# Performance work log

Hardware: AMD Instinct MI355X
Metric: run time of the kernel (lower is better)

Reference implementation:

```python
import jax, jax.numpy as jnp
import numpy as np

H = 32          # num_attention_heads
HD = 128        # head_dim
HID = H * HD    # hidden_size = 4096
KB_LEN = 1024   # number of KB entries
TOPK = 128      # top_k_kb (dynamic_sparsify=True)
ROPE_THETA = 10000.0
PAD = -1000000000.0  # PADDING_VALUE


def rope_cos_sin(position_ids, head_dim, theta):
    inv_freq = 1.0 / (theta ** (jnp.arange(0, head_dim, 2, dtype=jnp.float32) / head_dim))
    freqs = position_ids.astype(jnp.float32)[..., None] * inv_freq  # [B,q,hd/2]
    emb = jnp.concatenate([freqs, freqs], axis=-1)                  # [B,q,hd]
    return jnp.cos(emb), jnp.sin(emb)


def rotate_half(x):
    half = x.shape[-1] // 2
    return jnp.concatenate([-x[..., half:], x[..., :half]], axis=-1)


def apply_rope(q, k, cos, sin):
    cos = cos[:, None]  # [B,1,q,hd]
    sin = sin[:, None]
    return q * cos + rotate_half(q) * sin, k * cos + rotate_half(k) * sin


def setup_inputs() -> dict:
    key = jax.random.key(0)
    ks = jax.random.split(key, 9)
    B, Q = 1, 2048
    w_scale = 0.02  # keep activations numerically sane
    hidden_states = jax.random.normal(ks[0], (B, Q, HID), jnp.float32)
    causal = jnp.where(jnp.tril(jnp.ones((Q, Q), bool)), 0.0, PAD).astype(jnp.float32)
    attention_mask = jnp.broadcast_to(causal[None, None], (B, 1, Q, Q))
    position_ids = jnp.broadcast_to(jnp.arange(Q)[None], (B, Q))
    kb_keys = jax.random.normal(ks[1], (KB_LEN, HID), jnp.float32)
    kb_values = jax.random.normal(ks[2], (KB_LEN, HID), jnp.float32)
    Wq = jax.random.normal(ks[3], (HID, HID), jnp.float32) * w_scale
    Wq2 = jax.random.normal(ks[4], (HID, HID), jnp.float32) * w_scale
    Wk = jax.random.normal(ks[5], (HID, HID), jnp.float32) * w_scale
    Wv = jax.random.normal(ks[6], (HID, HID), jnp.float32) * w_scale
    Wo = jax.random.normal(ks[7], (HID, HID), jnp.float32) * w_scale
    score_shift = jnp.zeros((H, 1), jnp.float32) - 3.0
    return {"hidden_states": hidden_states, "attention_mask": attention_mask,
            "position_ids": position_ids, "kb_keys": kb_keys, "kb_values": kb_values,
            "Wq": Wq, "Wq2": Wq2, "Wk": Wk, "Wv": Wv, "Wo": Wo,
            "score_shift": score_shift}


def kblam_attention(hidden_states, attention_mask, position_ids, kb_keys, kb_values,
                    Wq, Wq2, Wk, Wv, Wo, score_shift):
    B, Q, _ = hidden_states.shape
    scale = 1.0 / np.sqrt(HD)

    def heads(x):  # [B,Q,HID] -> [B,H,Q,HD]
        return x.reshape(B, Q, H, HD).transpose(0, 2, 1, 3)

    q = heads(hidden_states @ Wq.T)
    q2 = heads(hidden_states @ Wq2.T)   # second query head (used for KB top-k pruning)
    k = heads(hidden_states @ Wk.T)
    v = heads(hidden_states @ Wv.T)

    cos, sin = rope_cos_sin(position_ids, HD, ROPE_THETA)
    q, k = apply_rope(q, k, cos, sin)   # num_kv_groups == 1, repeat_kv is identity

    # --- KB path: [kb_len, H*HD] -> [B,H,kb_len,HD] ---
    kbk = jnp.broadcast_to(kb_keys.reshape(KB_LEN, H, HD).transpose(1, 0, 2)[None], (B, H, KB_LEN, HD))
    kbv = jnp.broadcast_to(kb_values.reshape(KB_LEN, H, HD).transpose(1, 0, 2)[None], (B, H, KB_LEN, HD))

    # prune_key_value (dynamic_sparsify): top-k KB rows by summed q2-scores
    aw2 = jnp.einsum('bhqd,bhkd->bhqk', q2, kbk) * scale          # [B,H,Q,KB_LEN]
    idx = jax.lax.stop_gradient(jax.lax.top_k(aw2.sum((1, 2)), TOPK)[1])  # [B,TOPK]
    gidx = jnp.broadcast_to(idx[:, None, :, None], (B, H, TOPK, HD))
    kbk = jnp.take_along_axis(kbk, gidx, axis=2)                  # [B,H,TOPK,HD]
    kbv = jnp.take_along_axis(kbv, gidx, axis=2)
    kb_len = TOPK

    k_all = jnp.concatenate([kbk, k], axis=2)                     # [B,H,kb_len+Q,HD]
    v_all = jnp.concatenate([kbv, v], axis=2)

    # kb attention mask: zeros, except fully-padded query rows get PADDING_VALUE
    padding_mask = jnp.all(attention_mask < 0, axis=-1, keepdims=True)  # [B,1,Q,1]
    kb_mask = jnp.where(padding_mask, PAD, 0.0).astype(attention_mask.dtype)
    mask = jnp.concatenate([jnp.broadcast_to(kb_mask, (B, 1, Q, kb_len)), attention_mask], axis=-1)

    attn = jnp.einsum('bhqd,bhkd->bhqk', q, k_all) * scale
    # learned per-head shift on KB scores (score_shift: [H,1], init -3)
    attn = attn.at[..., :kb_len].add(score_shift.reshape(1, H, 1, 1))
    attn = attn + mask
    attn = jax.nn.softmax(attn.astype(jnp.float32), axis=-1).astype(q.dtype)

    out = jnp.einsum('bhqk,bhkd->bhqd', attn, v_all)              # [B,H,Q,HD]
    out = out.transpose(0, 2, 1, 3).reshape(B, Q, HID)
    return out @ Wo.T


def reference(hidden_states, attention_mask, position_ids, kb_keys, kb_values,
              Wq, Wq2, Wk, Wv, Wo, score_shift):
    return kblam_attention(hidden_states, attention_mask, position_ids, kb_keys, kb_values,
                           Wq, Wq2, Wk, Wv, Wo, score_shift)
```

## Files before the change

### kernel.cpp

```cpp
#include <hip/hip_runtime.h>
#include <stdint.h>
#include <stddef.h>

#define NH 32
#define HD 128
#define HID 4096
#define QLEN 2048
#define KBLEN 1024
#define NTOPK 128
#define KVLEN 2176
#define PADV -1e9f
#define SCALE 0.08838834764831845f
#define LOG2E 1.4426950408889634f
#define SC2 (SCALE * LOG2E)
#define DEFER_THR 8.0f

typedef __attribute__((ext_vector_type(4))) float f32x4;
typedef __attribute__((ext_vector_type(4))) unsigned short u16x4;
typedef __attribute__((ext_vector_type(8))) short s16x8;

typedef const __attribute__((address_space(1))) void* gas1_t;
typedef __attribute__((address_space(3))) void* las3_t;

__device__ __forceinline__ void gload_lds16(const void* g, void* l) {
  __builtin_amdgcn_global_load_lds((gas1_t)g, (las3_t)l, 16, 0, 0);
}

__device__ __forceinline__ unsigned short f2bf(float x) {
  union { float f; unsigned u; } z; z.f = x;
  unsigned r = z.u + 0x7fffu + ((z.u >> 16) & 1u);
  return (unsigned short)(r >> 16);
}


__global__ void k_cast(const float* __restrict__ src, unsigned short* __restrict__ dst, int n4) {
  int i = blockIdx.x * 256 + threadIdx.x;
  if (i >= n4) return;
  f32x4 v = ((const f32x4*)src)[i];
  u16x4 o;
  o[0] = f2bf(v[0]); o[1] = f2bf(v[1]); o[2] = f2bf(v[2]); o[3] = f2bf(v[3]);
  ((u16x4*)dst)[i] = o;
}

__global__ void k_rowsum_p(const float* __restrict__ x, float* __restrict__ part) {
  int d = blockIdx.x * 256 + threadIdx.x;
  int q0 = blockIdx.y * 128;
  float acc = 0.f;
  for (int q = q0; q < q0 + 128; ++q) acc += x[(size_t)q * HID + d];
  part[(size_t)blockIdx.y * HID + d] = acc;
}
__global__ void k_rowsum_r(const float* __restrict__ part, float* __restrict__ out) {
  int d = blockIdx.x * 256 + threadIdx.x;
  float acc = 0.f;
#pragma unroll
  for (int i = 0; i < 16; ++i) acc += part[(size_t)i * HID + d];
  out[d] = acc;
}

__global__ void k_dotrows(const float* __restrict__ vec, const float* __restrict__ mat,
                          float* __restrict__ out, int K, float s) {
  int n = blockIdx.x * 4 + (threadIdx.x >> 6);
  int lane = threadIdx.x & 63;
  const float* row = mat + (size_t)n * K;
  float acc = 0.f;
  for (int j = lane; j < K; j += 64) acc += vec[j] * row[j];
#pragma unroll
  for (int off = 32; off > 0; off >>= 1) acc += __shfl_down(acc, off, 64);
  if (lane == 0) out[n] = acc * s;
}

__global__ void k_topk(const float* __restrict__ scores, int* __restrict__ idx) {
  __shared__ float s[KBLEN];
  int t = threadIdx.x;
  s[t] = scores[t];
  __syncthreads();
  float mine = s[t];
  int rank = 0;
  for (int j = 0; j < KBLEN; ++j) {
    float v = s[j];
    rank += (v > mine) || (v == mine && j < t);
  }
  if (rank < NTOPK) idx[rank] = t;
}

__global__ void k_cs(const int* __restrict__ pos_ids, float2* __restrict__ cs) {
  int t = blockIdx.x * 256 + threadIdx.x;
  int p = t >> 6, i = t & 63;
  float pos = (float)pos_ids[p];
  float invf = powf(10000.0f, -(float)i / 64.0f);
  float a = pos * invf;
  cs[p * 64 + i] = make_float2(cosf(a), sinf(a));
}

__global__ void k_gather(const float* __restrict__ kbk, const float* __restrict__ kbv,
                         const int* __restrict__ idx,
                         unsigned short* __restrict__ kall, unsigned short* __restrict__ vallT) {
  int t = blockIdx.x * 256 + threadIdx.x;
  int d = t & 127;
  int i = (t >> 7) & 127;
  int hh = t >> 14;
  int kr = idx[i];
  size_t src = (size_t)kr * HID + hh * HD + d;
  kall[((size_t)hh * KVLEN + i) * HD + d] = f2bf(kbk[src]);
  vallT[((size_t)hh * HD + d) * KVLEN + i] = f2bf(kbv[src]);
}

#define GBK 64
#define ABUF 8192
#define BBUF 16384
#define BUFE (ABUF + BBUF)

template<int MODE>
__global__ __launch_bounds__(512)
void gemm_bt(const unsigned short* __restrict__ A, const unsigned short* __restrict__ B,
             float* __restrict__ Cf, unsigned short* __restrict__ Cb,
             int M, int N, int K, int RH, int RO, const float2* __restrict__ cs2) {
  __shared__ unsigned short lds[3 * BUFE];
  const int tid = threadIdx.x;
  const int lane = tid & 63;
  const int wave = tid >> 6;
  const int lo = lane & 15, hi = lane >> 4;
  const int wm = wave >> 2, wn = wave & 3;

  const int nwg = gridDim.x * gridDim.y;
  const int orig = blockIdx.y * gridDim.x + blockIdx.x;
  const int wg = (orig & 7) * (nwg >> 3) + (orig >> 3);
  const int bx = wg % gridDim.x, by = wg / gridDim.x;
  const int m0 = by * 128, n0 = bx * 256;

  auto stageA = [&](int kt, int bufe, int g) {
    int j0 = g * 512 + wave * 64;
    int j = j0 + lane;
    int row = j >> 3, cb = j & 7;
    gload_lds16(A + (size_t)(m0 + row) * K + kt * GBK + ((cb ^ (row & 7)) << 3),
                (void*)(lds + bufe + j0 * 8));
  };
  auto stageB = [&](int kt, int bufe, int g) {
    int j0 = g * 512 + wave * 64;
    int j = j0 + lane;
    int row = j >> 3, cb = j & 7;
    gload_lds16(B + (size_t)(n0 + row) * K + kt * GBK + ((cb ^ (row & 7)) << 3),
                (void*)(lds + bufe + ABUF + j0 * 8));
  };

  f32x4 acc[4][4] = {};

  stageA(0, 0, 0); stageA(0, 0, 1);
  stageB(0, 0, 0); stageB(0, 0, 1); stageB(0, 0, 2); stageB(0, 0, 3);
  stageA(1, BUFE, 0); stageA(1, BUFE, 1);
  stageB(1, BUFE, 0); stageB(1, BUFE, 1); stageB(1, BUFE, 2); stageB(1, BUFE, 3);

  const int NT = K / GBK;
  const int sa = (lo & 7) << 3;
  const int bbase = (wn >> 1) * 128 + (wn & 1) * 32;
  int bi = 0;

  for (int kt = 0; kt < NT; ++kt) {
    if (kt < NT - 1) { asm volatile("s_waitcnt vmcnt(6)" ::: "memory"); }
    else             { asm volatile("s_waitcnt vmcnt(0)" ::: "memory"); }
    __builtin_amdgcn_sched_barrier(0);
    __builtin_amdgcn_s_barrier();
    __builtin_amdgcn_sched_barrier(0);

    const int bufe = bi * BUFE;
    const int nbufe = ((bi + 2 >= 3) ? bi - 1 : bi + 2) * BUFE;
    const bool pre = (kt + 2 < NT);
    const unsigned short* Ab = lds + bufe;
    const unsigned short* Bb = lds + bufe + ABUF;
    const int arow = wm * 64 + lo;
    const int brow = bbase + lo;

    s16x8 af[4], b01[2], b23[2];
    const int c0 = (hi * 8) ^ sa;
    const int c1 = (32 + hi * 8) ^ sa;

#pragma unroll
    for (int i = 0; i < 4; ++i) af[i] = *(const s16x8*)(Ab + (arow + i * 16) * 64 + c0);
    b01[0] = *(const s16x8*)(Bb + (brow +  0) * 64 + c0);
    b01[1] = *(const s16x8*)(Bb + (brow + 16) * 64 + c0);
    if (pre) { stageA(kt + 2, nbufe, 0); stageA(kt + 2, nbufe, 1); }
    asm volatile("s_waitcnt lgkmcnt(0)" ::: "memory");
    __builtin_amdgcn_sched_barrier(0);
    __builtin_amdgcn_s_setprio(1);
#pragma unroll
    for (int i = 0; i < 4; ++i) {
      acc[i][0] = __builtin_amdgcn_mfma_f32_16x16x32_bf16(af[i], b01[0], acc[i][0], 0, 0, 0);
      acc[i][1] = __builtin_amdgcn_mfma_f32_16x16x32_bf16(af[i], b01[1], acc[i][1], 0, 0, 0);
    }
    __builtin_amdgcn_s_setprio(0);

    b23[0] = *(const s16x8*)(Bb + (brow + 64) * 64 + c0);
    b23[1] = *(const s16x8*)(Bb + (brow + 80) * 64 + c0);
    if (pre) { stageB(kt + 2, nbufe, 0); stageB(kt + 2, nbufe, 1); }
    asm volatile("s_waitcnt lgkmcnt(0)" ::: "memory");
    __builtin_amdgcn_sched_barrier(0);
    __builtin_amdgcn_s_setprio(1);
#pragma unroll
    for (int i = 0; i < 4; ++i) {
      acc[i][2] = __builtin_amdgcn_mfma_f32_16x16x32_bf16(af[i], b23[0], acc[i][2], 0, 0, 0);
      acc[i][3] = __builtin_amdgcn_mfma_f32_16x16x32_bf16(af[i], b23[1], acc[i][3], 0, 0, 0);
    }
    __builtin_amdgcn_s_setprio(0);

#pragma unroll
    for (int i = 0; i < 4; ++i) af[i] = *(const s16x8*)(Ab + (arow + i * 16) * 64 + c1);
    b01[0] = *(const s16x8*)(Bb + (brow +  0) * 64 + c1);
    b01[1] = *(const s16x8*)(Bb + (brow + 16) * 64 + c1);
    if (pre) { stageB(kt + 2, nbufe, 2); stageB(kt + 2, nbufe, 3); }
    asm volatile("s_waitcnt lgkmcnt(0)" ::: "memory");
    __builtin_amdgcn_sched_barrier(0);
    __builtin_amdgcn_s_setprio(1);
#pragma unroll
    for (int i = 0; i < 4; ++i) {
      acc[i][0] = __builtin_amdgcn_mfma_f32_16x16x32_bf16(af[i], b01[0], acc[i][0], 0, 0, 0);
      acc[i][1] = __builtin_amdgcn_mfma_f32_16x16x32_bf16(af[i], b01[1], acc[i][1], 0, 0, 0);
    }
    __builtin_amdgcn_s_setprio(0);

    b23[0] = *(const s16x8*)(Bb + (brow + 64) * 64 + c1);
    b23[1] = *(const s16x8*)(Bb + (brow + 80) * 64 + c1);
    asm volatile("s_waitcnt lgkmcnt(0)" ::: "memory");
    __builtin_amdgcn_sched_barrier(0);
    __builtin_amdgcn_s_setprio(1);
#pragma unroll
    for (int i = 0; i < 4; ++i) {
      acc[i][2] = __builtin_amdgcn_mfma_f32_16x16x32_bf16(af[i], b23[0], acc[i][2], 0, 0, 0);
      acc[i][3] = __builtin_amdgcn_mfma_f32_16x16x32_bf16(af[i], b23[1], acc[i][3], 0, 0, 0);
    }
    __builtin_amdgcn_s_setprio(0);

    bi = (bi + 1 == 3) ? 0 : bi + 1;
  }

  if (MODE == 2) {
#pragma unroll
    for (int i = 0; i < 4; ++i) {
#pragma unroll
      for (int j = 0; j < 2; ++j) {
#pragma unroll
        for (int r = 0; r < 4; ++r) {
          int row = m0 + wm * 64 + i * 16 + hi * 4 + r;
          int col = n0 + bbase + j * 16 + lo;
          int hh = col >> 7, d = col & 127;
          float2 cp = cs2[row * 64 + d];
          float x1 = acc[i][j][r], x2 = acc[i][j + 2][r];
          size_t base = ((size_t)hh * RH + RO + row) * HD;
          Cb[base + d]      = f2bf(x1 * cp.x - x2 * cp.y);
          Cb[base + d + 64] = f2bf(x2 * cp.x + x1 * cp.y);
        }
      }
    }
  } else if (MODE == 3) {
#pragma unroll
    for (int i = 0; i < 4; ++i) {
#pragma unroll
      for (int j = 0; j < 4; ++j) {
        int rowb = m0 + wm * 64 + i * 16 + hi * 4;
        int col = n0 + bbase + (j >> 1) * 64 + (j & 1) * 16 + lo;
        int hh = col >> 7, d = col & 127;
        u16x4 o4;
#pragma unroll
        for (int r = 0; r < 4; ++r) o4[r] = f2bf(acc[i][j][r]);
        *(u16x4*)(Cb + ((size_t)hh * HD + d) * RH + RO + rowb) = o4;
      }
    }
  } else {
#pragma unroll
    for (int i = 0; i < 4; ++i) {
#pragma unroll
      for (int j = 0; j < 4; ++j) {
#pragma unroll
        for (int r = 0; r < 4; ++r) {
          int row = m0 + wm * 64 + i * 16 + hi * 4 + r;
          int col = n0 + bbase + (j >> 1) * 64 + (j & 1) * 16 + lo;
          float v = acc[i][j][r];
          if (MODE == 0) {
            Cf[(size_t)row * N + col] = v;
          } else {
            int hh = col >> 7, d = col & 127;
            Cb[((size_t)hh * RH + RO + row) * HD + d] = f2bf(v);
          }
        }
      }
    }
  }
}

__global__ __launch_bounds__(256)
void attn_kernel(const unsigned short* __restrict__ qh,
                 const unsigned short* __restrict__ kall,
                 const unsigned short* __restrict__ vallT,
                 const float* __restrict__ sshift,
                 unsigned short* __restrict__ ctx) {
  __shared__ __align__(1024) unsigned short Ks[64 * 128];
  __shared__ __align__(1024) unsigned short Vs[128 * 64];
  __shared__ __align__(16)  unsigned short Plds[4][16 * 72];

  int orig = blockIdx.y * 16 + blockIdx.x;
  int wgid = (orig & 7) * 64 + (orig >> 3);
  int h = wgid >> 4;
  int xch = wgid & 15;

  const int tid = threadIdx.x;
  const int lane = tid & 63;
  const int wave = tid >> 6;
  const int lo = lane & 15;
  const int hi = lane >> 4;
  const float shiftL = sshift[h] * LOG2E;

  const unsigned short* kb = kall + (size_t)h * KVLEN * HD;
  const unsigned short* vtb = vallT + (size_t)h * HD * KVLEN;

#pragma unroll 1
  for (int half = 0; half < 2; ++half) {
    const int qc = half ? (31 - xch) : xch;
    const int m0 = qc * 64;

    s16x8 qf[4];
    {
      const unsigned short* qp = qh + ((size_t)h * QLEN + m0 + wave * 16 + lo) * HD + hi * 8;
#pragma unroll
      for (int kc = 0; kc < 4; ++kc) qf[kc] = *(const s16x8*)(qp + kc * 32);
    }

    float m_run[4], l_run[4];
#pragma unroll
    for (int r = 0; r < 4; ++r) { m_run[r] = -1e30f; l_run[r] = 0.f; }
    f32x4 o[8] = {};

    const int nt = qc + 3;
    const int qrow = m0 + wave * 16 + hi * 4;

    for (int kt = 0; kt < nt; ++kt) {
      const unsigned short* kg = kb + (size_t)kt * 64 * HD;
      const unsigned short* vg = vtb + kt * 64;
      __syncthreads();
#pragma unroll
      for (int it = 0; it < 4; ++it) {
        int j0 = it * 256 + wave * 64;
        int j = j0 + lane;
        int row = j >> 4, cb = j & 15;
        gload_lds16(kg + row * 128 + ((cb ^ (row & 7)) * 8), (void*)(Ks + j0 * 8));
        int d = j >> 3, c = j & 7;
        gload_lds16(vg + (size_t)d * KVLEN + ((c ^ (d & 7)) << 3), (void*)(Vs + j0 * 8));
      }
      __syncthreads();

      f32x4 s[4] = {};
#pragma unroll
      for (int kc = 0; kc < 4; ++kc) {
#pragma unroll
        for (int g = 0; g < 4; ++g) {
          int key = g * 16 + lo;
          s16x8 kf = *(const s16x8*)(Ks + key * 128 + (((kc * 4 + hi) ^ (key & 7)) * 8));
          s[g] = __builtin_amdgcn_mfma_f32_16x16x32_bf16(qf[kc], kf, s[g], 0, 0, 0);
        }
      }

      const int kvbase = kt * 64;
      float sv[4][4], mx[4];
#pragma unroll
      for (int r = 0; r < 4; ++r) {
        int qr = qrow + r;
#pragma unroll
        for (int g = 0; g < 4; ++g) {
          int kv = kvbase + g * 16 + lo;
          float v = s[g][r] * SC2;
          v = (kv < NTOPK) ? (v + shiftL) : ((kv - NTOPK > qr) ? PADV : v);
          sv[g][r] = v;
        }
        mx[r] = fmaxf(fmaxf(sv[0][r], sv[1][r]), fmaxf(sv[2][r], sv[3][r]));
      }
#pragma unroll
      for (int off = 1; off < 16; off <<= 1)
#pragma unroll
        for (int r = 0; r < 4; ++r) mx[r] = fmaxf(mx[r], __shfl_xor(mx[r], off, 64));

      bool need = false;
#pragma unroll
      for (int r = 0; r < 4; ++r) need = need || (mx[r] > m_run[r] + DEFER_THR);
      if (need) {
#pragma unroll
        for (int r = 0; r < 4; ++r) {
          float mn = fmaxf(m_run[r], mx[r]);
          float alpha = __builtin_amdgcn_exp2f(m_run[r] - mn);
          m_run[r] = mn;
          l_run[r] *= alpha;
#pragma unroll
          for (int db = 0; db < 8; ++db) o[db][r] *= alpha;
        }
      }

      float rs[4];
#pragma unroll
      for (int r = 0; r < 4; ++r) {
        float acc = 0.f;
#pragma unroll
        for (int g = 0; g < 4; ++g) {
          float p = __builtin_amdgcn_exp2f(sv[g][r] - m_run[r]);
          acc += p;
          Plds[wave][(hi * 4 + r) * 72 + g * 16 + lo] = f2bf(p);
        }
        rs[r] = acc;
      }
#pragma unroll
      for (int off = 1; off < 16; off <<= 1)
#pragma unroll
        for (int r = 0; r < 4; ++r) rs[r] += __shfl_xor(rs[r], off, 64);
#pragma unroll
      for (int r = 0; r < 4; ++r) l_run[r] += rs[r];

      s16x8 pf0 = *(const s16x8*)(&Plds[wave][lo * 72 + hi * 8]);
      s16x8 pf1 = *(const s16x8*)(&Plds[wave][lo * 72 + 32 + hi * 8]);
#pragma unroll
      for (int db = 0; db < 8; ++db) {
        int d = db * 16 + lo;
        s16x8 vf0 = *(const s16x8*)(Vs + d * 64 + ((hi       ^ (d & 7)) << 3));
        s16x8 vf1 = *(const s16x8*)(Vs + d * 64 + (((4 + hi) ^ (d & 7)) << 3));
        o[db] = __builtin_amdgcn_mfma_f32_16x16x32_bf16(pf0, vf0, o[db], 0, 0, 0);
        o[db] = __builtin_amdgcn_mfma_f32_16x16x32_bf16(pf1, vf1, o[db], 0, 0, 0);
      }
    }

#pragma unroll
    for (int db = 0; db < 8; ++db) {
#pragma unroll
      for (int r = 0; r < 4; ++r) {
        int row = qrow + r;
        int col = h * HD + db * 16 + lo;
        ctx[(size_t)row * HID + col] = f2bf(o[db][r] / l_run[r]);
      }
    }
  }
}


extern "C" void kernel_launch(void* const* d_in, const int* in_sizes, int n_in,
                              void* d_out, int out_size, void* d_ws, size_t ws_size,
                              hipStream_t stream) {
  const float* hidden    = (const float*)d_in[0];
  const int*   pos       = (const int*)d_in[2];
  const float* kb_keys   = (const float*)d_in[3];
  const float* kb_values = (const float*)d_in[4];
  const float* Wq        = (const float*)d_in[5];
  const float* Wq2       = (const float*)d_in[6];
  const float* Wk        = (const float*)d_in[7];
  const float* Wv        = (const float*)d_in[8];
  const float* Wo        = (const float*)d_in[9];
  const float* sshift    = (const float*)d_in[10];
  float* out = (float*)d_out;

  char* ws = (char*)d_ws;
  size_t off = 0;
  auto alloc = [&](size_t bytes) { char* p = ws + off; off += (bytes + 255) & ~(size_t)255; return p; };
  unsigned short* hidden_bf = (unsigned short*)alloc((size_t)QLEN * HID * 2);
  unsigned short* wbuf      = (unsigned short*)alloc((size_t)HID * HID * 2);
  unsigned short* qbf       = (unsigned short*)alloc((size_t)NH * QLEN * HD * 2);
  unsigned short* kallp     = (unsigned short*)alloc((size_t)NH * KVLEN * HD * 2);
  unsigned short* vallT     = (unsigned short*)alloc((size_t)NH * HD * KVLEN * 2);
  unsigned short* ctx       = (unsigned short*)alloc((size_t)QLEN * HID * 2);
  float2*         cs2       = (float2*)alloc((size_t)QLEN * 64 * 8);
  float*          part      = (float*)alloc((size_t)16 * HID * 4);
  float*          hsum      = (float*)alloc(HID * 4);
  float*          qs        = (float*)alloc(HID * 4);
  float*          scores    = (float*)alloc(KBLEN * 4);
  int*            idx       = (int*)alloc(NTOPK * 4);

  dim3 blk(256);

  k_cast<<<QLEN * HID / 4 / 256, blk, 0, stream>>>(hidden, hidden_bf, QLEN * HID / 4);
  k_rowsum_p<<<dim3(HID / 256, 16), blk, 0, stream>>>(hidden, part);
  k_rowsum_r<<<HID / 256, blk, 0, stream>>>(part, hsum);
  k_dotrows<<<HID / 4, blk, 0, stream>>>(hsum, Wq2, qs, HID, 1.0f);
  k_dotrows<<<KBLEN / 4, blk, 0, stream>>>(qs, kb_keys, scores, HID, SCALE);
  k_topk<<<1, KBLEN, 0, stream>>>(scores, idx);
  k_cs<<<QLEN * 64 / 256, blk, 0, stream>>>(pos, cs2);

  dim3 ggrid(HID / 256, QLEN / 128);
  dim3 gblk(512);
  int wcast_blocks = HID * HID / 4 / 256;

  k_cast<<<wcast_blocks, blk, 0, stream>>>(Wq, wbuf, HID * HID / 4);
  gemm_bt<2><<<ggrid, gblk, 0, stream>>>(hidden_bf, wbuf, nullptr, qbf, QLEN, HID, HID, QLEN, 0, cs2);
  k_cast<<<wcast_blocks, blk, 0, stream>>>(Wk, wbuf, HID * HID / 4);
  gemm_bt<2><<<ggrid, gblk, 0, stream>>>(hidden_bf, wbuf, nullptr, kallp, QLEN, HID, HID, KVLEN, NTOPK, cs2);
  k_cast<<<wcast_blocks, blk, 0, stream>>>(Wv, wbuf, HID * HID / 4);
  gemm_bt<3><<<ggrid, gblk, 0, stream>>>(hidden_bf, wbuf, nullptr, vallT, QLEN, HID, HID, KVLEN, NTOPK, cs2);

  k_gather<<<NH * NTOPK * HD / 256, blk, 0, stream>>>(kb_keys, kb_values, idx, kallp, vallT);

  dim3 agrid(16, NH);
  attn_kernel<<<agrid, blk, 0, stream>>>(qbf, kallp, vallT, sshift, ctx);

  k_cast<<<wcast_blocks, blk, 0, stream>>>(Wo, wbuf, HID * HID / 4);
  gemm_bt<0><<<ggrid, gblk, 0, stream>>>(ctx, wbuf, out, nullptr, QLEN, HID, HID, 0, 0, cs2);
}
```

Measured before the change: 570.3 us.

## Fold softmax scale into Q projection, one q-chunk per block, lighter attention inner loop

The attention scale and log2e are folded into the Q projection epilogue, so the attention loop no longer multiplies every score. The attention grid now launches one block per 64-row query chunk, with heaviest chunks first, instead of pairing light and heavy chunks in one block. Causal masking is applied only on the last tile, and the KB shift only on the first two tiles. The row-sum shuffle reduction moves out of the loop to the end, and the max-reduction shuffles run only when some lane needs a rescale (__any). This cuts per-tile ALU and shuffle work and improves load balance, at the cost of twice as many blocks and of rounding Q to bf16 after scaling.

```diff
diff --git a/kernel.cpp b/kernel.cpp
--- a/kernel.cpp
+++ b/kernel.cpp
@@ -114,7 +114,8 @@
 __global__ __launch_bounds__(512)
 void gemm_bt(const unsigned short* __restrict__ A, const unsigned short* __restrict__ B,
              float* __restrict__ Cf, unsigned short* __restrict__ Cb,
-             int M, int N, int K, int RH, int RO, const float2* __restrict__ cs2) {
+             int M, int N, int K, int RH, int RO, const float2* __restrict__ cs2,
+             float qsc) {
   __shared__ unsigned short lds[3 * BUFE];
   const int tid = threadIdx.x;
   const int lane = tid & 63;
@@ -243,7 +244,7 @@
           int col = n0 + bbase + j * 16 + lo;
           int hh = col >> 7, d = col & 127;
           float2 cp = cs2[row * 64 + d];
-          float x1 = acc[i][j][r], x2 = acc[i][j + 2][r];
+          float x1 = acc[i][j][r] * qsc, x2 = acc[i][j + 2][r] * qsc;
           size_t base = ((size_t)hh * RH + RO + row) * HD;
           Cb[base + d]      = f2bf(x1 * cp.x - x2 * cp.y);
           Cb[base + d + 64] = f2bf(x2 * cp.x + x1 * cp.y);
@@ -296,10 +297,10 @@
   __shared__ __align__(1024) unsigned short Vs[128 * 64];
   __shared__ __align__(16)  unsigned short Plds[4][16 * 72];
 
-  int orig = blockIdx.y * 16 + blockIdx.x;
-  int wgid = (orig & 7) * 64 + (orig >> 3);
-  int h = wgid >> 4;
-  int xch = wgid & 15;
+  int orig = blockIdx.y * 32 + blockIdx.x;
+  int wgid = (orig & 7) * 128 + (orig >> 3);
+  int h = wgid >> 5;
+  int qc = 31 - (wgid & 31);
 
   const int tid = threadIdx.x;
   const int lane = tid & 63;
@@ -311,125 +312,127 @@
   const unsigned short* kb = kall + (size_t)h * KVLEN * HD;
   const unsigned short* vtb = vallT + (size_t)h * HD * KVLEN;
 
-#pragma unroll 1
-  for (int half = 0; half < 2; ++half) {
-    const int qc = half ? (31 - xch) : xch;
-    const int m0 = qc * 64;
-
-    s16x8 qf[4];
-    {
-      const unsigned short* qp = qh + ((size_t)h * QLEN + m0 + wave * 16 + lo) * HD + hi * 8;
-#pragma unroll
-      for (int kc = 0; kc < 4; ++kc) qf[kc] = *(const s16x8*)(qp + kc * 32);
-    }
-
-    float m_run[4], l_run[4];
-#pragma unroll
-    for (int r = 0; r < 4; ++r) { m_run[r] = -1e30f; l_run[r] = 0.f; }
-    f32x4 o[8] = {};
-
-    const int nt = qc + 3;
-    const int qrow = m0 + wave * 16 + hi * 4;
-
-    for (int kt = 0; kt < nt; ++kt) {
-      const unsigned short* kg = kb + (size_t)kt * 64 * HD;
-      const unsigned short* vg = vtb + kt * 64;
-      __syncthreads();
-#pragma unroll
-      for (int it = 0; it < 4; ++it) {
-        int j0 = it * 256 + wave * 64;
-        int j = j0 + lane;
-        int row = j >> 4, cb = j & 15;
-        gload_lds16(kg + row * 128 + ((cb ^ (row & 7)) * 8), (void*)(Ks + j0 * 8));
-        int d = j >> 3, c = j & 7;
-        gload_lds16(vg + (size_t)d * KVLEN + ((c ^ (d & 7)) << 3), (void*)(Vs + j0 * 8));
-      }
-      __syncthreads();
-
-      f32x4 s[4] = {};
-#pragma unroll
-      for (int kc = 0; kc < 4; ++kc) {
-#pragma unroll
-        for (int g = 0; g < 4; ++g) {
-          int key = g * 16 + lo;
-          s16x8 kf = *(const s16x8*)(Ks + key * 128 + (((kc * 4 + hi) ^ (key & 7)) * 8));
-          s[g] = __builtin_amdgcn_mfma_f32_16x16x32_bf16(qf[kc], kf, s[g], 0, 0, 0);
-        }
-      }
-
+  const int m0 = qc * 64;
+  const int nt = qc + 3;
+  const int qrow = m0 + wave * 16 + hi * 4;
+
+  s16x8 qf[4];
+  {
+    const unsigned short* qp = qh + ((size_t)h * QLEN + m0 + wave * 16 + lo) * HD + hi * 8;
+#pragma unroll
+    for (int kc = 0; kc < 4; ++kc) qf[kc] = *(const s16x8*)(qp + kc * 32);
+  }
+
+  float m_run[4], l_part[4];
+#pragma unroll
+  for (int r = 0; r < 4; ++r) { m_run[r] = -1e30f; l_part[r] = 0.f; }
+  f32x4 o[8] = {};
+
+  for (int kt = 0; kt < nt; ++kt) {
+    const unsigned short* kg = kb + (size_t)kt * 64 * HD;
+    const unsigned short* vg = vtb + kt * 64;
+    __syncthreads();
+#pragma unroll
+    for (int it = 0; it < 4; ++it) {
+      int j0 = it * 256 + wave * 64;
+      int j = j0 + lane;
+      int row = j >> 4, cb = j & 15;
+      gload_lds16(kg + row * 128 + ((cb ^ (row & 7)) * 8), (void*)(Ks + j0 * 8));
+      int d = j >> 3, c = j & 7;
+      gload_lds16(vg + (size_t)d * KVLEN + ((c ^ (d & 7)) << 3), (void*)(Vs + j0 * 8));
+    }
+    __syncthreads();
+
+    f32x4 s[4] = {};
+#pragma unroll
+    for (int kc = 0; kc < 4; ++kc) {
+#pragma unroll
+      for (int g = 0; g < 4; ++g) {
+        int key = g * 16 + lo;
+        s16x8 kf = *(const s16x8*)(Ks + key * 128 + (((kc * 4 + hi) ^ (key & 7)) * 8));
+        s[g] = __builtin_amdgcn_mfma_f32_16x16x32_bf16(qf[kc], kf, s[g], 0, 0, 0);
+      }
+    }
+
+    if (kt < 2) {
+#pragma unroll
+      for (int g = 0; g < 4; ++g)
+#pragma unroll
+        for (int r = 0; r < 4; ++r) s[g][r] += shiftL;
+    } else if (kt == nt - 1) {
       const int kvbase = kt * 64;
-      float sv[4][4], mx[4];
 #pragma unroll
       for (int r = 0; r < 4; ++r) {
         int qr = qrow + r;
 #pragma unroll
         for (int g = 0; g < 4; ++g) {
           int kv = kvbase + g * 16 + lo;
-          float v = s[g][r] * SC2;
-          v = (kv < NTOPK) ? (v + shiftL) : ((kv - NTOPK > qr) ? PADV : v);
-          sv[g][r] = v;
+          s[g][r] = (kv - NTOPK > qr) ? PADV : s[g][r];
         }
-        mx[r] = fmaxf(fmaxf(sv[0][r], sv[1][r]), fmaxf(sv[2][r], sv[3][r]));
-      }
+      }
+    }
+
+    float mx[4];
+    bool need = false;
+#pragma unroll
+    for (int r = 0; r < 4; ++r) {
+      mx[r] = fmaxf(fmaxf(s[0][r], s[1][r]), fmaxf(s[2][r], s[3][r]));
+      need = need || (mx[r] > m_run[r] + DEFER_THR);
+    }
+    if (__any((int)need)) {
 #pragma unroll
       for (int off = 1; off < 16; off <<= 1)
 #pragma unroll
         for (int r = 0; r < 4; ++r) mx[r] = fmaxf(mx[r], __shfl_xor(mx[r], off, 64));
-
-      bool need = false;
-#pragma unroll
-      for (int r = 0; r < 4; ++r) need = need || (mx[r] > m_run[r] + DEFER_THR);
-      if (need) {
-#pragma unroll
-        for (int r = 0; r < 4; ++r) {
-          float mn = fmaxf(m_run[r], mx[r]);
-          float alpha = __builtin_amdgcn_exp2f(m_run[r] - mn);
-          m_run[r] = mn;
-          l_run[r] *= alpha;
-#pragma unroll
-          for (int db = 0; db < 8; ++db) o[db][r] *= alpha;
-        }
-      }
-
-      float rs[4];
 #pragma unroll
       for (int r = 0; r < 4; ++r) {
-        float acc = 0.f;
-#pragma unroll
-        for (int g = 0; g < 4; ++g) {
-          float p = __builtin_amdgcn_exp2f(sv[g][r] - m_run[r]);
-          acc += p;
-          Plds[wave][(hi * 4 + r) * 72 + g * 16 + lo] = f2bf(p);
-        }
-        rs[r] = acc;
-      }
-#pragma unroll
-      for (int off = 1; off < 16; off <<= 1)
-#pragma unroll
-        for (int r = 0; r < 4; ++r) rs[r] += __shfl_xor(rs[r], off, 64);
-#pragma unroll
-      for (int r = 0; r < 4; ++r) l_run[r] += rs[r];
-
-      s16x8 pf0 = *(const s16x8*)(&Plds[wave][lo * 72 + hi * 8]);
-      s16x8 pf1 = *(const s16x8*)(&Plds[wave][lo * 72 + 32 + hi * 8]);
-#pragma unroll
-      for (int db = 0; db < 8; ++db) {
-        int d = db * 16 + lo;
-        s16x8 vf0 = *(const s16x8*)(Vs + d * 64 + ((hi       ^ (d & 7)) << 3));
-        s16x8 vf1 = *(const s16x8*)(Vs + d * 64 + (((4 + hi) ^ (d & 7)) << 3));
-        o[db] = __builtin_amdgcn_mfma_f32_16x16x32_bf16(pf0, vf0, o[db], 0, 0, 0);
-        o[db] = __builtin_amdgcn_mfma_f32_16x16x32_bf16(pf1, vf1, o[db], 0, 0, 0);
-      }
-    }
-
+        float mn = fmaxf(m_run[r], mx[r]);
+        float alpha = __builtin_amdgcn_exp2f(m_run[r] - mn);
+        m_run[r] = mn;
+        l_part[r] *= alpha;
+#pragma unroll
+        for (int db = 0; db < 8; ++db) o[db][r] *= alpha;
+      }
+    }
+
+#pragma unroll
+    for (int r = 0; r < 4; ++r) {
+#pragma unroll
+      for (int g = 0; g < 4; ++g) {
+        float p = __builtin_amdgcn_exp2f(s[g][r] - m_run[r]);
+        l_part[r] += p;
+        Plds[wave][(hi * 4 + r) * 72 + g * 16 + lo] = f2bf(p);
+      }
+    }
+
+    s16x8 pf0 = *(const s16x8*)(&Plds[wave][lo * 72 + hi * 8]);
+    s16x8 pf1 = *(const s16x8*)(&Plds[wave][lo * 72 + 32 + hi * 8]);
 #pragma unroll
     for (int db = 0; db < 8; ++db) {
-#pragma unroll
-      for (int r = 0; r < 4; ++r) {
-        int row = qrow + r;
-        int col = h * HD + db * 16 + lo;
-        ctx[(size_t)row * HID + col] = f2bf(o[db][r] / l_run[r]);
-      }
+      int d = db * 16 + lo;
+      s16x8 vf0 = *(const s16x8*)(Vs + d * 64 + ((hi       ^ (d & 7)) << 3));
+      s16x8 vf1 = *(const s16x8*)(Vs + d * 64 + (((4 + hi) ^ (d & 7)) << 3));
+      o[db] = __builtin_amdgcn_mfma_f32_16x16x32_bf16(pf0, vf0, o[db], 0, 0, 0);
+      o[db] = __builtin_amdgcn_mfma_f32_16x16x32_bf16(pf1, vf1, o[db], 0, 0, 0);
+    }
+  }
+
+#pragma unroll
+  for (int off = 1; off < 16; off <<= 1)
+#pragma unroll
+    for (int r = 0; r < 4; ++r) l_part[r] += __shfl_xor(l_part[r], off, 64);
+
+  float rinv[4];
+#pragma unroll
+  for (int r = 0; r < 4; ++r) rinv[r] = __builtin_amdgcn_rcpf(l_part[r]);
+
+#pragma unroll
+  for (int db = 0; db < 8; ++db) {
+#pragma unroll
+    for (int r = 0; r < 4; ++r) {
+      int row = qrow + r;
+      int col = h * HD + db * 16 + lo;
+      ctx[(size_t)row * HID + col] = f2bf(o[db][r] * rinv[r]);
     }
   }
 }
@@ -481,17 +484,17 @@
   int wcast_blocks = HID * HID / 4 / 256;
 
   k_cast<<<wcast_blocks, blk, 0, stream>>>(Wq, wbuf, HID * HID / 4);
-  gemm_bt<2><<<ggrid, gblk, 0, stream>>>(hidden_bf, wbuf, nullptr, qbf, QLEN, HID, HID, QLEN, 0, cs2);
+  gemm_bt<2><<<ggrid, gblk, 0, stream>>>(hidden_bf, wbuf, nullptr, qbf, QLEN, HID, HID, QLEN, 0, cs2, (float)SC2);
   k_cast<<<wcast_blocks, blk, 0, stream>>>(Wk, wbuf, HID * HID / 4);
-  gemm_bt<2><<<ggrid, gblk, 0, stream>>>(hidden_bf, wbuf, nullptr, kallp, QLEN, HID, HID, KVLEN, NTOPK, cs2);
+  gemm_bt<2><<<ggrid, gblk, 0, stream>>>(hidden_bf, wbuf, nullptr, kallp, QLEN, HID, HID, KVLEN, NTOPK, cs2, 1.0f);
   k_cast<<<wcast_blocks, blk, 0, stream>>>(Wv, wbuf, HID * HID / 4);
-  gemm_bt<3><<<ggrid, gblk, 0, stream>>>(hidden_bf, wbuf, nullptr, vallT, QLEN, HID, HID, KVLEN, NTOPK, cs2);
+  gemm_bt<3><<<ggrid, gblk, 0, stream>>>(hidden_bf, wbuf, nullptr, vallT, QLEN, HID, HID, KVLEN, NTOPK, cs2, 1.0f);
 
   k_gather<<<NH * NTOPK * HD / 256, blk, 0, stream>>>(kb_keys, kb_values, idx, kallp, vallT);
 
-  dim3 agrid(16, NH);
+  dim3 agrid(32, NH);
   attn_kernel<<<agrid, blk, 0, stream>>>(qbf, kallp, vallT, sshift, ctx);
 
   k_cast<<<wcast_blocks, blk, 0, stream>>>(Wo, wbuf, HID * HID / 4);
-  gemm_bt<0><<<ggrid, gblk, 0, stream>>>(ctx, wbuf, out, nullptr, QLEN, HID, HID, 0, 0, cs2);
-}
+  gemm_bt<0><<<ggrid, gblk, 0, stream>>>(ctx, wbuf, out, nullptr, QLEN, HID, HID, 0, 0, cs2, 1.0f);
+}
```

Measured after the change: 566.3 us (median of 2 runs). Within noise of the previous version (-0.7%).
